# Optimization experiments

Hardware: AMD Instinct MI355X
Metric: run time of the kernel (lower is better)

## Reference

```python
import jax, jax.numpy as jnp
import numpy as np


def setup_inputs() -> dict:
    key = jax.random.key(0)
    k1, k2, k3, k4 = jax.random.split(key, 4)
    N, F, E = 100000, 128, 1600000
    Fo = F // 2
    x = jax.random.normal(k1, (N, F), dtype=jnp.float32)
    edge_index = jax.random.randint(k2, (2, E), 0, N, dtype=jnp.int32)
    W_conv = jax.random.normal(k3, (Fo, F), dtype=jnp.float32) * (1.0 / np.sqrt(F))
    b_conv = jnp.zeros((Fo,), dtype=jnp.float32)
    W_lin = jax.random.normal(k4, (1, Fo), dtype=jnp.float32) * (1.0 / np.sqrt(Fo))
    b_lin = jnp.zeros((1,), dtype=jnp.float32)
    return {"x": x, "edge_index": edge_index, "W_conv": W_conv,
            "b_conv": b_conv, "W_lin": W_lin, "b_lin": b_lin}


def gcn_conv(x, edge_index, W_conv, b_conv):
    # PyG GCNConv: add self-loops, symmetric normalization, x@W.T, scatter-add, + bias
    N = x.shape[0]
    loops = jnp.arange(N, dtype=edge_index.dtype)
    src = jnp.concatenate([edge_index[0], loops])  # message sources
    dst = jnp.concatenate([edge_index[1], loops])  # aggregation targets
    h = x @ W_conv.T  # [N, Fo]
    deg = jax.ops.segment_sum(jnp.ones_like(dst, dtype=h.dtype), dst, num_segments=N)
    dinv = jnp.where(deg > 0, jax.lax.rsqrt(deg), 0.0)
    norm = dinv[src] * dinv[dst]  # [E+N]
    msg = h[src] * norm[:, None]  # [E+N, Fo] -- dominant memory traffic
    agg = jax.ops.segment_sum(msg, dst, num_segments=N)
    return agg + b_conv


def reference(x, edge_index, W_conv, b_conv, W_lin, b_lin):
    h = gcn_conv(x, edge_index, W_conv, b_conv)
    h = jax.nn.relu(h)
    logits = h @ W_lin.T + b_lin  # [N, 1]
    return jax.nn.sigmoid(logits)
```

## Files before the change

### kernel.cpp

```cpp
#include <hip/hip_runtime.h>
#include <math.h>

#define F_IN   128
#define F_OUT  64
#define CHUNK  8192
#define MAXB   512

typedef short bf16x8 __attribute__((ext_vector_type(8)));
typedef float f32x4  __attribute__((ext_vector_type(4)));

__device__ __forceinline__ float bf2f(unsigned short u) {
    union { unsigned int i; float f; } c; c.i = ((unsigned int)u) << 16; return c.f;
}
__device__ __forceinline__ unsigned short f2bf(float f) {
    union { float f; unsigned int i; } c; c.f = f;
    unsigned int r = c.i + 0x7FFFu + ((c.i >> 16) & 1u);
    return (unsigned short)(r >> 16);
}

__global__ __launch_bounds__(256) void k_hist(
    const int* __restrict__ dst, int E, int* __restrict__ M, int NBLK, int NBC) {
    __shared__ int hist[MAXB];
    for (int c = threadIdx.x; c < MAXB; c += 256) hist[c] = 0;
    __syncthreads();
    int e0 = blockIdx.x * CHUNK;
    int e1 = min(E, e0 + CHUNK);
    for (int e = e0 + threadIdx.x; e < e1; e += 256)
        atomicAdd(&hist[dst[e] >> 8], 1);
    __syncthreads();
    for (int c = threadIdx.x; c < NBC; c += 256)
        M[c * NBLK + blockIdx.x] = hist[c];
}

__global__ void k_scan1(const int* __restrict__ M, int* __restrict__ tmp,
                        int* __restrict__ bsum, int S) {
    __shared__ int sh[256];
    int i = blockIdx.x * 256 + threadIdx.x;
    int v = (i < S) ? M[i] : 0;
    sh[threadIdx.x] = v;
    __syncthreads();
    for (int off = 1; off < 256; off <<= 1) {
        int t = (threadIdx.x >= off) ? sh[threadIdx.x - off] : 0;
        __syncthreads();
        sh[threadIdx.x] += t;
        __syncthreads();
    }
    if (i < S) tmp[i] = sh[threadIdx.x];
    if (threadIdx.x == 255) bsum[blockIdx.x] = sh[255];
}

__global__ void k_scan2(int* __restrict__ bsum, int NB1) {
    __shared__ int sh[512];
    int v = (threadIdx.x < NB1) ? bsum[threadIdx.x] : 0;
    sh[threadIdx.x] = v;
    __syncthreads();
    for (int off = 1; off < 512; off <<= 1) {
        int t = (threadIdx.x >= off) ? sh[threadIdx.x - off] : 0;
        __syncthreads();
        sh[threadIdx.x] += t;
        __syncthreads();
    }
    if (threadIdx.x < NB1) bsum[threadIdx.x] = sh[threadIdx.x] - v;
}

__global__ void k_scan3(int* __restrict__ M, const int* __restrict__ tmp,
                        const int* __restrict__ bsum, int* __restrict__ bucketOff,
                        int* __restrict__ offsets,
                        int S, int NBLK, int NBC, int N, int E) {
    int i = blockIdx.x * 256 + threadIdx.x;
    if (i < S) {
        int orig = M[i];
        int o = tmp[i] - orig + bsum[blockIdx.x];
        M[i] = o;
        if (i % NBLK == 0) bucketOff[i / NBLK] = o;
    }
    if (i == 0) { bucketOff[NBC] = E; offsets[N] = E; }
}

__global__ __launch_bounds__(256) void k_scatter(
    const int* __restrict__ src, const int* __restrict__ dst, int E,
    const int* __restrict__ M, int NBLK, int NBC, unsigned int* __restrict__ entries) {
    __shared__ int cur[MAXB];
    for (int c = threadIdx.x; c < NBC; c += 256)
        cur[c] = M[c * NBLK + blockIdx.x];
    __syncthreads();
    int e0 = blockIdx.x * CHUNK;
    int e1 = min(E, e0 + CHUNK);
    for (int e = e0 + threadIdx.x; e < e1; e += 256) {
        int d = dst[e];
        int s = src[e];
        int p = atomicAdd(&cur[d >> 8], 1);
        entries[p] = ((unsigned int)(d & 255) << 24) | (unsigned int)s;
    }
}

__global__ __launch_bounds__(256) void k_sort(
    const unsigned int* __restrict__ entries, const int* __restrict__ bucketOff,
    int* __restrict__ offsets, int* __restrict__ srcs, int N) {
    __shared__ int hist[256];
    __shared__ int curs[256];
    const int tid = threadIdx.x;
    const int b = blockIdx.x;
    const int start = bucketOff[b];
    const int end   = bucketOff[b + 1];

    hist[tid] = 0;
    __syncthreads();
    for (int i = start + tid; i < end; i += 256)
        atomicAdd(&hist[entries[i] >> 24], 1);
    __syncthreads();

    int cntv = hist[tid];
    curs[tid] = cntv;
    __syncthreads();
    for (int off = 1; off < 256; off <<= 1) {
        int t = (tid >= off) ? curs[tid - off] : 0;
        __syncthreads();
        curs[tid] += t;
        __syncthreads();
    }
    int excl = curs[tid] - cntv;
    int d = (b << 8) + tid;
    if (d < N) offsets[d] = start + excl;
    __syncthreads();
    curs[tid] = start + excl;
    __syncthreads();

    for (int i = start + tid; i < end; i += 256) {
        unsigned int v = entries[i];
        int p = atomicAdd(&curs[v >> 24], 1);
        srcs[p] = (int)(v & 0xFFFFFFu);
    }
}

__global__ __launch_bounds__(256) void k_gemm(
    const float* __restrict__ x, const float* __restrict__ W,
    const int* __restrict__ offsets, unsigned short* __restrict__ g, int N) {
    __shared__ unsigned short xs[64 * F_IN];
    __shared__ unsigned short Wsh[F_OUT * F_IN];
    __shared__ float dinvs[64];

    const int tid  = threadIdx.x;
    const int row0 = blockIdx.x * 64;

    {
        const float4* W4 = (const float4*)W;
        #pragma unroll
        for (int t = 0; t < 8; ++t) {
            int idx = t * 256 + tid;
            float4 v = W4[idx];
            ushort4 u;
            u.x = f2bf(v.x); u.y = f2bf(v.y); u.z = f2bf(v.z); u.w = f2bf(v.w);
            *(ushort4*)&Wsh[idx * 4] = u;
        }
    }
    {
        const float4* x4 = (const float4*)x;
        #pragma unroll
        for (int t = 0; t < 8; ++t) {
            int idx = t * 256 + tid;
            int r = idx >> 5;
            int grow = row0 + r;
            float4 v = make_float4(0.f, 0.f, 0.f, 0.f);
            if (grow < N) v = x4[(size_t)grow * 32 + (idx & 31)];
            ushort4 u;
            u.x = f2bf(v.x); u.y = f2bf(v.y); u.z = f2bf(v.z); u.w = f2bf(v.w);
            *(ushort4*)&xs[idx * 4] = u;
        }
    }
    if (tid < 64) {
        int grow = row0 + tid;
        float dv = 1.0f;
        if (grow < N) dv = rsqrtf((float)(offsets[grow + 1] - offsets[grow]) + 1.0f);
        dinvs[tid] = dv;
    }
    __syncthreads();

    const int lane = tid & 63;
    const int wave = tid >> 6;
    const int m = lane & 15;
    const int q = lane >> 4;
    const int r0 = wave * 16;

    bf16x8 a[4];
    #pragma unroll
    for (int ks = 0; ks < 4; ++ks)
        a[ks] = *(const bf16x8*)&xs[(r0 + m) * F_IN + ks * 32 + q * 8];

    f32x4 acc[4] = {{0,0,0,0},{0,0,0,0},{0,0,0,0},{0,0,0,0}};
    #pragma unroll
    for (int ct = 0; ct < 4; ++ct) {
        #pragma unroll
        for (int ks = 0; ks < 4; ++ks) {
            bf16x8 b = *(const bf16x8*)&Wsh[(ct * 16 + m) * F_IN + ks * 32 + q * 8];
            acc[ct] = __builtin_amdgcn_mfma_f32_16x16x32_bf16(a[ks], b, acc[ct], 0, 0, 0);
        }
    }

    float dv[4];
    #pragma unroll
    for (int reg = 0; reg < 4; ++reg)
        dv[reg] = dinvs[r0 + q * 4 + reg];
    #pragma unroll
    for (int ct = 0; ct < 4; ++ct) {
        #pragma unroll
        for (int reg = 0; reg < 4; ++reg) {
            int grow = row0 + r0 + q * 4 + reg;
            if (grow < N)
                g[(size_t)grow * F_OUT + ct * 16 + m] = f2bf(acc[ct][reg] * dv[reg]);
        }
    }
}

__global__ __launch_bounds__(256) void k_pull(
    const unsigned short* __restrict__ g, const int* __restrict__ offsets,
    const int* __restrict__ srcs, const float* __restrict__ b_conv,
    const float* __restrict__ W_lin, const float* __restrict__ b_lin,
    float* __restrict__ out, int N) {
    const int lane   = threadIdx.x & 63;
    const int wave   = (blockIdx.x * blockDim.x + threadIdx.x) >> 6;
    const int nwaves = (gridDim.x * blockDim.x) >> 6;
    const float wl = W_lin[lane];
    const float bb = b_conv[lane];
    const float bl = b_lin[0];

    for (int i = wave; i < N; i += nwaves) {
        int e0 = __builtin_amdgcn_readfirstlane(offsets[i]);
        int e1 = __builtin_amdgcn_readfirstlane(offsets[i + 1]);
        float acc = bf2f(g[(size_t)i * F_OUT + lane]);
        int e = e0;
        for (; e + 8 <= e1; e += 8) {
            int s0 = srcs[e + 0], s1 = srcs[e + 1], s2 = srcs[e + 2], s3 = srcs[e + 3];
            int s4 = srcs[e + 4], s5 = srcs[e + 5], s6 = srcs[e + 6], s7 = srcs[e + 7];
            float v0 = bf2f(g[(size_t)s0 * F_OUT + lane]);
            float v1 = bf2f(g[(size_t)s1 * F_OUT + lane]);
            float v2 = bf2f(g[(size_t)s2 * F_OUT + lane]);
            float v3 = bf2f(g[(size_t)s3 * F_OUT + lane]);
            float v4 = bf2f(g[(size_t)s4 * F_OUT + lane]);
            float v5 = bf2f(g[(size_t)s5 * F_OUT + lane]);
            float v6 = bf2f(g[(size_t)s6 * F_OUT + lane]);
            float v7 = bf2f(g[(size_t)s7 * F_OUT + lane]);
            acc += ((v0 + v1) + (v2 + v3)) + ((v4 + v5) + (v6 + v7));
        }
        for (; e < e1; ++e)
            acc += bf2f(g[(size_t)srcs[e] * F_OUT + lane]);

        float dinv = rsqrtf((float)(e1 - e0) + 1.0f);
        float a = fmaxf(acc * dinv + bb, 0.f);
        float t = a * wl;
        #pragma unroll
        for (int off = 32; off > 0; off >>= 1)
            t += __shfl_down(t, off, 64);
        if (lane == 0)
            out[i] = 1.0f / (1.0f + expf(-(t + bl)));
    }
}

extern "C" void kernel_launch(void* const* d_in, const int* in_sizes, int n_in,
                              void* d_out, int out_size, void* d_ws, size_t ws_size,
                              hipStream_t stream) {
    const float* x      = (const float*)d_in[0];
    const int*   ei     = (const int*)d_in[1];
    const float* W_conv = (const float*)d_in[2];
    const float* b_conv = (const float*)d_in[3];
    const float* W_lin  = (const float*)d_in[4];
    const float* b_lin  = (const float*)d_in[5];

    const int N = in_sizes[0] / F_IN;
    const int E = in_sizes[1] / 2;
    const int* src = ei;
    const int* dst = ei + E;
    float* out = (float*)d_out;

    const int NBC  = (N + 255) >> 8;
    const int NBLK = (E + CHUNK - 1) / CHUNK;
    const int S    = NBC * NBLK;
    const int NB1  = (S + 255) / 256;

    const int Na = (N + 256) & ~255;
    const int Sa = (S + 256) & ~255;
    const int Ea = (E + 255) & ~255;

    int* M         = (int*)d_ws;
    int* tmp       = M + Sa;
    int* bsum      = tmp + Sa;
    int* bucketOff = bsum + 512;
    int* offsets   = bucketOff + ((NBC + 257) & ~255);
    unsigned int* entries = (unsigned int*)(offsets + Na);
    int* srcs      = (int*)(entries + Ea);
    unsigned short* g = (unsigned short*)(srcs + Ea);

    k_hist   <<<NBLK, 256, 0, stream>>>(dst, E, M, NBLK, NBC);
    k_scan1  <<<NB1, 256, 0, stream>>>(M, tmp, bsum, S);
    k_scan2  <<<1, 512, 0, stream>>>(bsum, NB1);
    k_scan3  <<<NB1, 256, 0, stream>>>(M, tmp, bsum, bucketOff, offsets, S, NBLK, NBC, N, E);
    k_scatter<<<NBLK, 256, 0, stream>>>(src, dst, E, M, NBLK, NBC, entries);
    k_sort   <<<NBC, 256, 0, stream>>>(entries, bucketOff, offsets, srcs, N);
    k_gemm   <<<(N + 63) / 64, 256, 0, stream>>>(x, W_conv, offsets, g, N);
    k_pull   <<<4096, 256, 0, stream>>>(g, offsets, srcs, b_conv, W_lin, b_lin, out, N);
}
```

Baseline: 202.5 us.

## Split wave into two half-waves gathering separate edges with 32-bit loads

Result: faster. 198.2 us (-2.1%).

```diff
diff --git a/kernel.cpp b/kernel.cpp
--- a/kernel.cpp
+++ b/kernel.cpp
@@ -3,7 +3,7 @@
 
 #define F_IN   128
 #define F_OUT  64
-#define CHUNK  8192
+#define CHUNK  5120
 #define MAXB   512
 
 typedef short bf16x8 __attribute__((ext_vector_type(8)));
@@ -218,41 +218,68 @@
     const float* __restrict__ W_lin, const float* __restrict__ b_lin,
     float* __restrict__ out, int N) {
     const int lane   = threadIdx.x & 63;
+    const int li     = lane & 31;
+    const int half   = lane >> 5;
     const int wave   = (blockIdx.x * blockDim.x + threadIdx.x) >> 6;
     const int nwaves = (gridDim.x * blockDim.x) >> 6;
-    const float wl = W_lin[lane];
-    const float bb = b_conv[lane];
-    const float bl = b_lin[0];
+
+    const float2 wl = ((const float2*)W_lin)[li];
+    const float2 bb = ((const float2*)b_conv)[li];
+    const float  bl = b_lin[0];
+    const unsigned int* g32 = (const unsigned int*)g;
 
     for (int i = wave; i < N; i += nwaves) {
         int e0 = __builtin_amdgcn_readfirstlane(offsets[i]);
         int e1 = __builtin_amdgcn_readfirstlane(offsets[i + 1]);
-        float acc = bf2f(g[(size_t)i * F_OUT + lane]);
+
+        unsigned int us = g32[(size_t)i * 32 + li];
+        float a0 = half ? 0.f : bf2f((unsigned short)(us & 0xFFFFu));
+        float a1 = half ? 0.f : bf2f((unsigned short)(us >> 16));
+
         int e = e0;
-        for (; e + 8 <= e1; e += 8) {
-            int s0 = srcs[e + 0], s1 = srcs[e + 1], s2 = srcs[e + 2], s3 = srcs[e + 3];
-            int s4 = srcs[e + 4], s5 = srcs[e + 5], s6 = srcs[e + 6], s7 = srcs[e + 7];
-            float v0 = bf2f(g[(size_t)s0 * F_OUT + lane]);
-            float v1 = bf2f(g[(size_t)s1 * F_OUT + lane]);
-            float v2 = bf2f(g[(size_t)s2 * F_OUT + lane]);
-            float v3 = bf2f(g[(size_t)s3 * F_OUT + lane]);
-            float v4 = bf2f(g[(size_t)s4 * F_OUT + lane]);
-            float v5 = bf2f(g[(size_t)s5 * F_OUT + lane]);
-            float v6 = bf2f(g[(size_t)s6 * F_OUT + lane]);
-            float v7 = bf2f(g[(size_t)s7 * F_OUT + lane]);
-            acc += ((v0 + v1) + (v2 + v3)) + ((v4 + v5) + (v6 + v7));
-        }
-        for (; e < e1; ++e)
-            acc += bf2f(g[(size_t)srcs[e] * F_OUT + lane]);
+        int M16 = e0 + ((e1 - e0) & ~15);
+        for (; e < M16; e += 16) {
+            unsigned int u[8];
+            #pragma unroll
+            for (int t = 0; t < 8; ++t) {
+                int sA = srcs[e + 2 * t];
+                int sB = srcs[e + 2 * t + 1];
+                int s  = half ? sB : sA;
+                u[t] = g32[(size_t)s * 32 + li];
+            }
+            #pragma unroll
+            for (int t = 0; t < 8; ++t) {
+                a0 += bf2f((unsigned short)(u[t] & 0xFFFFu));
+                a1 += bf2f((unsigned short)(u[t] >> 16));
+            }
+        }
+        for (; e + 2 <= e1; e += 2) {
+            int sA = srcs[e];
+            int sB = srcs[e + 1];
+            int s  = half ? sB : sA;
+            unsigned int u = g32[(size_t)s * 32 + li];
+            a0 += bf2f((unsigned short)(u & 0xFFFFu));
+            a1 += bf2f((unsigned short)(u >> 16));
+        }
+        if (e < e1 && half == 0) {
+            int s = srcs[e];
+            unsigned int u = g32[(size_t)s * 32 + li];
+            a0 += bf2f((unsigned short)(u & 0xFFFFu));
+            a1 += bf2f((unsigned short)(u >> 16));
+        }
+
+        a0 += __shfl_xor(a0, 32, 64);
+        a1 += __shfl_xor(a1, 32, 64);
 
         float dinv = rsqrtf((float)(e1 - e0) + 1.0f);
-        float a = fmaxf(acc * dinv + bb, 0.f);
-        float t = a * wl;
+        float r0 = fmaxf(a0 * dinv + bb.x, 0.f);
+        float r1 = fmaxf(a1 * dinv + bb.y, 0.f);
+        float t = r0 * wl.x + r1 * wl.y;
         #pragma unroll
         for (int off = 32; off > 0; off >>= 1)
             t += __shfl_down(t, off, 64);
         if (lane == 0)
-            out[i] = 1.0f / (1.0f + expf(-(t + bl)));
+            out[i] = 1.0f / (1.0f + expf(-(0.5f * t + bl)));
     }
 }
 
```
